# Optimization experiments

Hardware: AMD Instinct MI355X
Metric: run time of the kernel (lower is better)

## Reference

```python
import jax, jax.numpy as jnp
import numpy as np

B, N, R, NF, NH = 2, 2048, 16384, 128, 3
PSTEP = 3


def _lin(x, w, b):
    return x @ w + b


def _mlp2(x, w0, b0, w1, b1):
    return jax.nn.relu(_lin(jax.nn.relu(_lin(x, w0, b0)), w1, b1))


def setup_inputs() -> dict:
    key = jax.random.key(0)
    ks = jax.random.split(key, 16)

    def w(k, i, o):
        return (jax.random.normal(k, (i, o), dtype=jnp.float32) / np.float32(np.sqrt(i)))

    a_cur = jax.random.uniform(ks[0], (B, N), dtype=jnp.float32)
    s_cur = jax.random.normal(ks[1], (B, N, 3), dtype=jnp.float32)
    s_delta = jax.random.normal(ks[2], (B, NH, N, 3), dtype=jnp.float32)
    # Rr/Rs: dense one-hot receiver/sender matrices (B, rel_num, N)
    Rr = jax.nn.one_hot(jax.random.randint(ks[3], (B, R), 0, N), N, dtype=jnp.float32)
    Rs = jax.nn.one_hot(jax.random.randint(ks[4], (B, R), 0, N), N, dtype=jnp.float32)
    edge_attrs = (jax.random.uniform(ks[5], (B, R, 1)) > 0.5).astype(jnp.float32)
    z = lambda n: jnp.zeros((n,), dtype=jnp.float32)
    return {
        "a_cur": a_cur, "s_cur": s_cur, "s_delta": s_delta,
        "Rr": Rr, "Rs": Rs, "edge_attrs": edge_attrs,
        "pe_w0": w(ks[6], 3 * NH + 1, NF), "pe_b0": z(NF),
        "pe_w1": w(ks[7], NF, NF), "pe_b1": z(NF),
        "re_w0": w(ks[8], 6, NF), "re_b0": z(NF),
        "re_w1": w(ks[9], NF, NF), "re_b1": z(NF),
        "re_w2": w(ks[10], NF, NF), "re_b2": z(NF),
        "rp_w": w(ks[11], 3 * NF, NF), "rp_b": z(NF),
        "pp_w": w(ks[12], 2 * NF, NF), "pp_b": z(NF),
        "pr_w0": w(ks[13], NF, NF), "pr_b0": z(NF),
        "pr_w1": w(ks[14], NF, 3), "pr_b1": z(3),
    }


def reference(a_cur, s_cur, s_delta, Rr, Rs, edge_attrs,
              pe_w0, pe_b0, pe_w1, pe_b1,
              re_w0, re_b0, re_w1, re_b1, re_w2, re_b2,
              rp_w, rp_b, pp_w, pp_b,
              pr_w0, pr_b0, pr_w1, pr_b1):
    b, nh, n, _ = s_delta.shape
    # (B, n_history, N, 3) -> (B, N, 3*n_history)
    s_delta_flat = jnp.transpose(s_delta, (0, 2, 1, 3)).reshape(b, n, -1)
    a_r = jnp.einsum('brn,bn->br', Rr, a_cur)[..., None]
    a_s = jnp.einsum('brn,bn->br', Rs, a_cur)[..., None]
    s_r = jnp.einsum('brn,bnd->brd', Rr, s_cur)
    s_s = jnp.einsum('brn,bnd->brd', Rs, s_cur)

    particle_encode = _mlp2(jnp.concatenate([s_delta_flat, a_cur[..., None]], -1),
                            pe_w0, pe_b0, pe_w1, pe_b1)
    rel_in = jnp.concatenate([a_r, a_s, s_r - s_s, edge_attrs], -1)
    relation_encode = jax.nn.relu(_lin(
        jax.nn.relu(_lin(jax.nn.relu(_lin(rel_in, re_w0, re_b0)), re_w1, re_b1)),
        re_w2, re_b2))

    effect = particle_encode
    for _ in range(PSTEP):
        e_r = jnp.einsum('brn,bnf->brf', Rr, effect)
        e_s = jnp.einsum('brn,bnf->brf', Rs, effect)
        e_rel = jax.nn.relu(_lin(jnp.concatenate([relation_encode, e_r, e_s], -1), rp_w, rp_b))
        agg = jnp.einsum('brn,brf->bnf', Rr, e_rel)  # Rr^T aggregation
        effect = jax.nn.relu(
            _lin(jnp.concatenate([particle_encode, agg], -1), pp_w, pp_b) + effect)

    pred = _lin(jax.nn.relu(_lin(effect, pr_w0, pr_b0)), pr_w1, pr_b1)
    return pred + s_cur
```

## Files before the change

kernel.cpp:

```cpp
#include <hip/hip_runtime.h>
#include <hip/hip_bf16.h>
#include <stdint.h>

#define B_ 2
#define N_ 2048
#define R_ 16384
#define NF_ 128
#define NH_ 3
#define PSTEP_ 3
#define EDGES (B_ * R_)
#define NODES (B_ * N_)
#define PREP_EXB0 1024

typedef _Float16 f16;
typedef _Float16 f16x4 __attribute__((ext_vector_type(4)));
typedef float f32x4 __attribute__((ext_vector_type(4)));

struct GemmLds { f16 Ah[128 * 128], Al[128 * 128], Bh[128 * 128], Bl[128 * 128]; };
struct VecLds {
  float wbuf[64][NF_];
  float xt[NF_][20];
  float ht[NF_][20];
  float w0s[10][NF_];
  float b0s[NF_], b1s[NF_];
  float xs[16][10];
  float w1s[NF_][4];
};
union MainLds { GemmLds g; VecLds v; };

__device__ __forceinline__ void gl16(const f16* g, f16* l) {
  typedef const __attribute__((address_space(1))) uint32_t* gas_t;
  typedef __attribute__((address_space(3))) uint32_t* las_t;
  __builtin_amdgcn_global_load_lds((gas_t)(const void*)g, (las_t)(void*)l, 16, 0, 0);
}

__device__ __forceinline__ void mfma_block(const f16* Ah, const f16* Al,
                                           const f16* Bh, const f16* Bl,
                                           f32x4 (&acc)[8][2], int lane, int w) {
  const int l16 = lane & 15, l4 = lane >> 4;
  #pragma unroll 1
  for (int kk = 0; kk < 8; ++kk) {
    const int c16 = kk * 2 + (l4 >> 1);
    const int sub = (l4 & 1) * 4;
    f16x4 bh[2], bl[2];
    #pragma unroll
    for (int nf = 0; nf < 2; ++nf) {
      const int n = w * 32 + nf * 16 + l16;
      const int off = n * 128 + ((c16 ^ (n & 7)) * 8) + sub;
      bh[nf] = *(const f16x4*)&Bh[off];
      bl[nf] = *(const f16x4*)&Bl[off];
    }
    #pragma unroll
    for (int m = 0; m < 8; ++m) {
      const int r = m * 16 + l16;
      const int off = r * 128 + ((c16 ^ (r & 7)) * 8) + sub;
      const f16x4 ah = *(const f16x4*)&Ah[off];
      const f16x4 al = *(const f16x4*)&Al[off];
      #pragma unroll
      for (int nf = 0; nf < 2; ++nf) {
        acc[m][nf] = __builtin_amdgcn_mfma_f32_16x16x16f16(ah, bh[nf], acc[m][nf], 0, 0, 0);
        acc[m][nf] = __builtin_amdgcn_mfma_f32_16x16x16f16(ah, bl[nf], acc[m][nf], 0, 0, 0);
        acc[m][nf] = __builtin_amdgcn_mfma_f32_16x16x16f16(al, bh[nf], acc[m][nf], 0, 0, 0);
      }
    }
  }
}

__device__ __forceinline__ void frags_to_lds(f32x4 (&acc)[8][2], f16* Ah, f16* Al,
                                             int lane, int w) {
  const int l16 = lane & 15, l4 = lane >> 4;
  #pragma unroll
  for (int m = 0; m < 8; ++m)
    #pragma unroll
    for (int nf = 0; nf < 2; ++nf)
      #pragma unroll
      for (int i = 0; i < 4; ++i) {
        const float v = fmaxf(acc[m][nf][i], 0.f);
        const int row = m * 16 + l4 * 4 + i;
        const int col = w * 32 + nf * 16 + l16;
        const int off = row * 128 + (((col >> 3) ^ (row & 7)) * 8) + (col & 7);
        const f16 h = (f16)v;
        Ah[off] = h; Al[off] = (f16)(v - (float)h);
      }
}

__global__ __launch_bounds__(256) void k_prep(
    const float* __restrict__ Rr, const float* __restrict__ Rs,
    const float* __restrict__ rp_w, const float* __restrict__ re_w1,
    const float* __restrict__ re_w2,
    int* __restrict__ recv, int* __restrict__ send,
    f16* __restrict__ rpT_h, f16* __restrict__ rpT_l,
    f16* __restrict__ re1T_h, f16* __restrict__ re1T_l,
    f16* __restrict__ re2T_h, f16* __restrict__ re2T_l,
    float4* __restrict__ agg4) {
  const int bid = blockIdx.x, t = threadIdx.x;
  if (bid < 512) {
    agg4[bid * 256 + t] = make_float4(0.f, 0.f, 0.f, 0.f);
  } else if (bid >= 513 && bid < 833) {
    const int i = (bid - 513) * 256 + t;
    const int S1 = 384 * 128, S2 = S1 + 128 * 128, S3 = S2 + 128 * 128;
    if (i < S1) {
      const int k = i >> 7, n = i & 127;
      const float v = rp_w[i];
      const f16 h = (f16)v;
      rpT_h[n * 384 + k] = h; rpT_l[n * 384 + k] = (f16)(v - (float)h);
    } else if (i < S2) {
      const int j = i - S1, k = j >> 7, n = j & 127;
      const float v = re_w1[j];
      const f16 h = (f16)v;
      re1T_h[n * 128 + k] = h; re1T_l[n * 128 + k] = (f16)(v - (float)h);
    } else if (i < S3) {
      const int j = i - S2, k = j >> 7, n = j & 127;
      const float v = re_w2[j];
      const f16 h = (f16)v;
      re2T_h[n * 128 + k] = h; re2T_l[n * 128 + k] = (f16)(v - (float)h);
    }
  } else if (bid >= PREP_EXB0) {
    const int wid = (bid - PREP_EXB0) * 4 + (t >> 6);
    const int lane = t & 63;
    const bool isR = wid < EDGES;
    const int row = isR ? wid : wid - EDGES;
    const float4* p = reinterpret_cast<const float4*>((isR ? Rr : Rs) + (size_t)row * N_);
    int found = 0;
    #pragma unroll 1
    for (int it = 0; it < N_ / 256; ++it) {
      const float4 v = p[it * 64 + lane];
      const int base = (it * 64 + lane) * 4;
      bool hit = false;
      if (v.x != 0.f) { found = base;     hit = true; }
      if (v.y != 0.f) { found = base + 1; hit = true; }
      if (v.z != 0.f) { found = base + 2; hit = true; }
      if (v.w != 0.f) { found = base + 3; hit = true; }
      if (__any(hit)) break;
    }
    #pragma unroll
    for (int off = 32; off > 0; off >>= 1)
      found = max(found, __shfl_down(found, off, 64));
    if (lane == 0) (isR ? recv : send)[row] = found;
  }
}

__global__ __launch_bounds__(256, 1) void k_pre(
    const float* __restrict__ a_cur, const float* __restrict__ s_cur,
    const float* __restrict__ s_delta, const float* __restrict__ ea,
    const int* __restrict__ recv, const int* __restrict__ send,
    const float* __restrict__ pe_w0, const float* __restrict__ pe_b0,
    const float* __restrict__ pe_w1, const float* __restrict__ pe_b1,
    const float* __restrict__ re_w0, const float* __restrict__ re_b0,
    const float* __restrict__ re_b1, const float* __restrict__ re_b2,
    const f16* __restrict__ re1T_h, const f16* __restrict__ re1T_l,
    const f16* __restrict__ re2T_h, const f16* __restrict__ re2T_l,
    float* __restrict__ pe, f16* __restrict__ pe_h, f16* __restrict__ pe_l,
    f16* __restrict__ rel_h, f16* __restrict__ rel_l) {
  __shared__ MainLds u;
  __shared__ float xt6[6][128];
  __shared__ float w0s6[6][128];
  __shared__ float sb0[128];

  const int bid = blockIdx.x, t = threadIdx.x;
  const int lane = t & 63, w = t >> 6;
  const int l16 = lane & 15, l4 = lane >> 4;
  const int f = t & 127, g = t >> 7;

  auto stageB = [&](const f16* gh, const f16* gl) {
    #pragma unroll
    for (int rb = 0; rb < 32; rb += 4) {
      const int r0w = w * 32 + rb;
      const int row = r0w + l4;
      const int sc = (l16 ^ (row & 7)) * 8;
      gl16(gh + (size_t)row * 128 + sc, &u.g.Bh[r0w * 128]);
      gl16(gl + (size_t)row * 128 + sc, &u.g.Bl[r0w * 128]);
    }
  };

  {
    const int r0 = bid * 16;
    for (int i = t; i < 10 * NF_; i += 256) u.v.w0s[i >> 7][i & 127] = pe_w0[i];
    if (t < NF_) { u.v.b0s[t] = pe_b0[t]; u.v.b1s[t] = pe_b1[t]; }
    for (int i = t; i < 160; i += 256) {
      const int r = i / 10, k = i % 10;
      const int gr = r0 + r, b = gr >> 11, n = gr & (N_ - 1);
      u.v.xs[r][k] = (k < 9)
          ? s_delta[(((size_t)b * NH_ + (k / 3)) * N_ + n) * 3 + (k % 3)]
          : a_cur[gr];
    }
    __syncthreads();
    for (int r = g * 8; r < g * 8 + 8; ++r) {
      float a1 = u.v.b0s[f];
      #pragma unroll
      for (int k = 0; k < 10; ++k) a1 = fmaf(u.v.xs[r][k], u.v.w0s[k][f], a1);
      u.v.ht[f][r] = fmaxf(a1, 0.f);
    }
    float acc[8];
    #pragma unroll
    for (int i = 0; i < 8; ++i) acc[i] = u.v.b1s[f];
    for (int h = 0; h < 2; ++h) {
      __syncthreads();
      for (int i = t; i < 64 * NF_; i += 256) u.v.wbuf[i >> 7][i & 127] = pe_w1[h * 64 * NF_ + i];
      __syncthreads();
      for (int k = 0; k < 64; ++k) {
        const float wv = u.v.wbuf[k][f];
        #pragma unroll
        for (int i = 0; i < 2; ++i) {
          const float4 x4 = *reinterpret_cast<const float4*>(&u.v.ht[h * 64 + k][g * 8 + i * 4]);
          acc[i*4+0] = fmaf(x4.x, wv, acc[i*4+0]);
          acc[i*4+1] = fmaf(x4.y, wv, acc[i*4+1]);
          acc[i*4+2] = fmaf(x4.z, wv, acc[i*4+2]);
          acc[i*4+3] = fmaf(x4.w, wv, acc[i*4+3]);
        }
      }
    }
    #pragma unroll
    for (int i = 0; i < 8; ++i) {
      const size_t idx = (size_t)(r0 + g * 8 + i) * NF_ + f;
      const float v = fmaxf(acc[i], 0.f);
      pe[idx] = v;
      const f16 h = (f16)v;
      pe_h[idx] = h; pe_l[idx] = (f16)(v - (float)h);
    }
  }
  __syncthreads();

  {
    const int e0 = bid * 128;
    if (t < 128) {
      const int ge = e0 + t, b = ge >> 14;
      const int rc = recv[ge], sd = send[ge];
      xt6[0][t] = a_cur[(b << 11) + rc];
      xt6[1][t] = a_cur[(b << 11) + sd];
      #pragma unroll
      for (int d = 0; d < 3; ++d)
        xt6[2 + d][t] = s_cur[(size_t)((b << 11) + rc) * 3 + d]
                      - s_cur[(size_t)((b << 11) + sd) * 3 + d];
      xt6[5][t] = ea[ge];
    }
    stageB(re1T_h, re1T_l);
    for (int i = t; i < 6 * 128; i += 256) w0s6[i >> 7][i & 127] = re_w0[i];
    if (t < 128) sb0[t] = re_b0[t];
    __syncthreads();
    {
      float wreg[6];
      #pragma unroll
      for (int k = 0; k < 6; ++k) wreg[k] = w0s6[k][f];
      const float b0v = sb0[f];
      for (int r = g * 64; r < g * 64 + 64; ++r) {
        float a1 = b0v;
        #pragma unroll
        for (int k = 0; k < 6; ++k) a1 = fmaf(xt6[k][r], wreg[k], a1);
        a1 = fmaxf(a1, 0.f);
        const int off = r * 128 + ((((f >> 3)) ^ (r & 7)) * 8) + (f & 7);
        const f16 h = (f16)a1;
        u.g.Ah[off] = h; u.g.Al[off] = (f16)(a1 - (float)h);
      }
    }
    __syncthreads();
    f32x4 acc[8][2];
    {
      const float bv0 = re_b1[w * 32 + l16], bv1 = re_b1[w * 32 + 16 + l16];
      #pragma unroll
      for (int m = 0; m < 8; ++m) {
        acc[m][0] = (f32x4){bv0, bv0, bv0, bv0};
        acc[m][1] = (f32x4){bv1, bv1, bv1, bv1};
      }
    }
    mfma_block(u.g.Ah, u.g.Al, u.g.Bh, u.g.Bl, acc, lane, w);
    __syncthreads();
    frags_to_lds(acc, u.g.Ah, u.g.Al, lane, w);
    stageB(re2T_h, re2T_l);
    {
      const float bv0 = re_b2[w * 32 + l16], bv1 = re_b2[w * 32 + 16 + l16];
      #pragma unroll
      for (int m = 0; m < 8; ++m) {
        acc[m][0] = (f32x4){bv0, bv0, bv0, bv0};
        acc[m][1] = (f32x4){bv1, bv1, bv1, bv1};
      }
    }
    __syncthreads();
    mfma_block(u.g.Ah, u.g.Al, u.g.Bh, u.g.Bl, acc, lane, w);
    __syncthreads();
    frags_to_lds(acc, u.g.Ah, u.g.Al, lane, w);
    __syncthreads();
    {
      const int row = t >> 1, hf = t & 1;
      const float4* sA = (const float4*)&u.g.Ah[row * 128 + hf * 64];
      const float4* sL = (const float4*)&u.g.Al[row * 128 + hf * 64];
      float4* dA = (float4*)&rel_h[(size_t)(e0 + row) * 128 + hf * 64];
      float4* dL = (float4*)&rel_l[(size_t)(e0 + row) * 128 + hf * 64];
      #pragma unroll
      for (int j = 0; j < 8; ++j) { dA[j] = sA[j]; dL[j] = sL[j]; }
    }
  }
}

__global__ __launch_bounds__(256, 1) void k_erel(
    const f16* __restrict__ rel_h, const f16* __restrict__ rel_l,
    const f16* __restrict__ src_h, const f16* __restrict__ src_l,
    const int* __restrict__ recv, const int* __restrict__ send,
    const f16* __restrict__ rpT_h, const f16* __restrict__ rpT_l,
    const float* __restrict__ rp_b, float* __restrict__ agg) {
  __shared__ GemmLds u;
  __shared__ int eidx0[128], eidx1[128];
  const int bid = blockIdx.x, t = threadIdx.x;
  const int lane = t & 63, w = t >> 6;
  const int l16 = lane & 15, l4 = lane >> 4;
  const int e0 = bid * 128;
  const int b = bid >> 7;
  if (t < 128) eidx0[t] = recv[e0 + t];
  else         eidx1[t - 128] = send[e0 + t - 128];
  f32x4 acc[8][2];
  {
    const float bv0 = rp_b[w * 32 + l16], bv1 = rp_b[w * 32 + 16 + l16];
    #pragma unroll
    for (int m = 0; m < 8; ++m) {
      acc[m][0] = (f32x4){bv0, bv0, bv0, bv0};
      acc[m][1] = (f32x4){bv1, bv1, bv1, bv1};
    }
  }
  #pragma unroll 1
  for (int ch = 0; ch < 3; ++ch) {
    __syncthreads();
    #pragma unroll
    for (int rb = 0; rb < 32; rb += 4) {
      const int r0w = w * 32 + rb;
      const int row = r0w + l4;
      const int ge = e0 + row;
      if (ch == 0) {
        gl16(rel_h + (size_t)ge * 128 + l16 * 8, &u.Ah[r0w * 128]);
        gl16(rel_l + (size_t)ge * 128 + l16 * 8, &u.Al[r0w * 128]);
      } else {
        const int node = (ch == 1) ? eidx0[row] : eidx1[row];
        const size_t ao = ((size_t)(b << 11) + node) * 128 + ((l16 ^ (row & 7)) * 8);
        gl16(src_h + ao, &u.Ah[r0w * 128]);
        gl16(src_l + ao, &u.Al[r0w * 128]);
      }
      const int sc = (l16 ^ (row & 7)) * 8;
      gl16(rpT_h + (size_t)row * 384 + ch * 128 + sc, &u.Bh[r0w * 128]);
      gl16(rpT_l + (size_t)row * 384 + ch * 128 + sc, &u.Bl[r0w * 128]);
    }
    __syncthreads();
    mfma_block(u.Ah, u.Al, u.Bh, u.Bl, acc, lane, w);
  }
  #pragma unroll
  for (int m = 0; m < 8; ++m)
    #pragma unroll
    for (int nf = 0; nf < 2; ++nf)
      #pragma unroll
      for (int i = 0; i < 4; ++i) {
        const float v = fmaxf(acc[m][nf][i], 0.f);
        const int row = m * 16 + l4 * 4 + i;
        const int col = w * 32 + nf * 16 + l16;
        const int rc = eidx0[row];
        atomicAdd(&agg[((size_t)(b << 11) + rc) * NF_ + col], v);
      }
}

__global__ __launch_bounds__(256) void k_update(
    const float* __restrict__ pe, float* __restrict__ agg,
    const float* __restrict__ src_f,
    const float* __restrict__ pp_w, const float* __restrict__ pp_b,
    float* __restrict__ dst_f, f16* __restrict__ dst_h, f16* __restrict__ dst_l) {
  __shared__ alignas(16) float wbuf[64][NF_];
  __shared__ alignas(16) float xt[NF_][20];
  const int t = threadIdx.x, f = t & 127, g = t >> 7;
  const int r0 = blockIdx.x * 16;
  float acc[8];
  {
    const float bias = pp_b[f];
    #pragma unroll
    for (int i = 0; i < 8; ++i) acc[i] = bias;
  }
  for (int c = 0; c < 2; ++c) {
    __syncthreads();
    {
      const int e = t >> 4, k0 = (t & 15) * 8;
      float* srcp = (float*)((c ? agg : pe) + (size_t)(r0 + e) * NF_ + k0);
      #pragma unroll
      for (int j = 0; j < 2; ++j) {
        const float4 v = *reinterpret_cast<const float4*>(srcp + j * 4);
        xt[k0 + j*4 + 0][e] = v.x;
        xt[k0 + j*4 + 1][e] = v.y;
        xt[k0 + j*4 + 2][e] = v.z;
        xt[k0 + j*4 + 3][e] = v.w;
      }
      if (c == 1) {
        #pragma unroll
        for (int j = 0; j < 2; ++j)
          *reinterpret_cast<float4*>(srcp + j * 4) = make_float4(0.f, 0.f, 0.f, 0.f);
      }
    }
    #pragma unroll 1
    for (int h = 0; h < 2; ++h) {
      __syncthreads();
      for (int i = t; i < 64 * NF_; i += 256)
        wbuf[i >> 7][i & 127] = pp_w[(size_t)(c * NF_ + h * 64) * NF_ + i];
      __syncthreads();
      for (int k = 0; k < 64; ++k) {
        const float wv = wbuf[k][f];
        const int ka = h * 64 + k;
        #pragma unroll
        for (int i = 0; i < 2; ++i) {
          const float4 x4 = *reinterpret_cast<const float4*>(&xt[ka][g * 8 + i * 4]);
          acc[i*4+0] = fmaf(x4.x, wv, acc[i*4+0]);
          acc[i*4+1] = fmaf(x4.y, wv, acc[i*4+1]);
          acc[i*4+2] = fmaf(x4.z, wv, acc[i*4+2]);
          acc[i*4+3] = fmaf(x4.w, wv, acc[i*4+3]);
        }
      }
    }
  }
  #pragma unroll
  for (int i = 0; i < 8; ++i) {
    const size_t idx = (size_t)(r0 + g * 8 + i) * NF_ + f;
    const float v = fmaxf(acc[i] + src_f[idx], 0.f);
    dst_f[idx] = v;
    const f16 h = (f16)v;
    dst_h[idx] = h; dst_l[idx] = (f16)(v - (float)h);
  }
}

__global__ __launch_bounds__(256) void k_predict(
    const float* __restrict__ eff, const float* __restrict__ s_cur,
    const float* __restrict__ w0, const float* __restrict__ b0,
    const float* __restrict__ w1, const float* __restrict__ b1,
    float* __restrict__ out) {
  __shared__ alignas(16) float wbuf[64][NF_];
  __shared__ alignas(16) float xt[NF_][20];
  __shared__ alignas(16) float ht[NF_][20];
  __shared__ float w1s[NF_][4];
  const int t = threadIdx.x, f = t & 127, g = t >> 7;
  const int r0 = blockIdx.x * 16;
  for (int i = t; i < NF_ * 3; i += 256) w1s[i / 3][i % 3] = w1[i];
  {
    const int e = t >> 4, k0 = (t & 15) * 8;
    const float* src = eff + (size_t)(r0 + e) * NF_ + k0;
    #pragma unroll
    for (int j = 0; j < 2; ++j) {
      const float4 v = *reinterpret_cast<const float4*>(src + j * 4);
      xt[k0 + j*4 + 0][e] = v.x;
      xt[k0 + j*4 + 1][e] = v.y;
      xt[k0 + j*4 + 2][e] = v.z;
      xt[k0 + j*4 + 3][e] = v.w;
    }
  }
  float acc[8];
  {
    const float bias = b0[f];
    #pragma unroll
    for (int i = 0; i < 8; ++i) acc[i] = bias;
  }
  for (int h = 0; h < 2; ++h) {
    __syncthreads();
    for (int i = t; i < 64 * NF_; i += 256) wbuf[i >> 7][i & 127] = w0[h * 64 * NF_ + i];
    __syncthreads();
    for (int k = 0; k < 64; ++k) {
      const float wv = wbuf[k][f];
      const int ka = h * 64 + k;
      #pragma unroll
      for (int i = 0; i < 2; ++i) {
        const float4 x4 = *reinterpret_cast<const float4*>(&xt[ka][g * 8 + i * 4]);
        acc[i*4+0] = fmaf(x4.x, wv, acc[i*4+0]);
        acc[i*4+1] = fmaf(x4.y, wv, acc[i*4+1]);
        acc[i*4+2] = fmaf(x4.z, wv, acc[i*4+2]);
        acc[i*4+3] = fmaf(x4.w, wv, acc[i*4+3]);
      }
    }
  }
  #pragma unroll
  for (int i = 0; i < 8; ++i) ht[f][g * 8 + i] = fmaxf(acc[i], 0.f);
  __syncthreads();
  if (t < 48) {
    const int r = t / 3, d = t % 3;
    float a2 = b1[d];
    for (int k = 0; k < NF_; ++k) a2 = fmaf(ht[k][r], w1s[k][d], a2);
    const int gr = r0 + r;
    out[(size_t)gr * 3 + d] = a2 + s_cur[(size_t)gr * 3 + d];
  }
}

extern "C" void kernel_launch(void* const* d_in, const int* in_sizes, int n_in,
                              void* d_out, int out_size, void* d_ws, size_t ws_size,
                              hipStream_t stream) {
  (void)in_sizes; (void)n_in; (void)out_size; (void)ws_size;
  const float* a_cur   = (const float*)d_in[0];
  const float* s_cur   = (const float*)d_in[1];
  const float* s_delta = (const float*)d_in[2];
  const float* Rr      = (const float*)d_in[3];
  const float* Rs      = (const float*)d_in[4];
  const float* ea      = (const float*)d_in[5];
  const float* pe_w0 = (const float*)d_in[6];
  const float* pe_b0 = (const float*)d_in[7];
  const float* pe_w1 = (const float*)d_in[8];
  const float* pe_b1 = (const float*)d_in[9];
  const float* re_w0 = (const float*)d_in[10];
  const float* re_b0 = (const float*)d_in[11];
  const float* re_w1 = (const float*)d_in[12];
  const float* re_b1 = (const float*)d_in[13];
  const float* re_w2 = (const float*)d_in[14];
  const float* re_b2 = (const float*)d_in[15];
  const float* rp_w  = (const float*)d_in[16];
  const float* rp_b  = (const float*)d_in[17];
  const float* pp_w  = (const float*)d_in[18];
  const float* pp_b  = (const float*)d_in[19];
  const float* pr_w0 = (const float*)d_in[20];
  const float* pr_b0 = (const float*)d_in[21];
  const float* pr_w1 = (const float*)d_in[22];
  const float* pr_b1 = (const float*)d_in[23];
  float* out = (float*)d_out;

  uint8_t* wp = (uint8_t*)d_ws;
  auto alloc = [&](size_t bytes) {
    void* p = (void*)wp;
    wp += (bytes + 255) & ~(size_t)255;
    return p;
  };
  int* recv   = (int*)alloc(EDGES * 4);
  int* send   = (int*)alloc(EDGES * 4);
  float* pe   = (float*)alloc((size_t)NODES * NF_ * 4);
  f16* pe_h   = (f16*)alloc((size_t)NODES * NF_ * 2);
  f16* pe_l   = (f16*)alloc((size_t)NODES * NF_ * 2);
  float* eff  = (float*)alloc((size_t)NODES * NF_ * 4);
  f16* eff_h  = (f16*)alloc((size_t)NODES * NF_ * 2);
  f16* eff_l  = (f16*)alloc((size_t)NODES * NF_ * 2);
  float* agg  = (float*)alloc((size_t)NODES * NF_ * 4);
  f16* rel_h  = (f16*)alloc((size_t)EDGES * NF_ * 2);
  f16* rel_l  = (f16*)alloc((size_t)EDGES * NF_ * 2);
  f16* rpT_h  = (f16*)alloc(128 * 384 * 2);
  f16* rpT_l  = (f16*)alloc(128 * 384 * 2);
  f16* re1T_h = (f16*)alloc(128 * 128 * 2);
  f16* re1T_l = (f16*)alloc(128 * 128 * 2);
  f16* re2T_h = (f16*)alloc(128 * 128 * 2);
  f16* re2T_l = (f16*)alloc(128 * 128 * 2);

  k_prep<<<PREP_EXB0 + (2 * EDGES) / 4, 256, 0, stream>>>(
      Rr, Rs, rp_w, re_w1, re_w2, recv, send,
      rpT_h, rpT_l, re1T_h, re1T_l, re2T_h, re2T_l, (float4*)agg);

  k_pre<<<256, 256, 0, stream>>>(
      a_cur, s_cur, s_delta, ea, recv, send,
      pe_w0, pe_b0, pe_w1, pe_b1, re_w0, re_b0, re_b1, re_b2,
      re1T_h, re1T_l, re2T_h, re2T_l,
      pe, pe_h, pe_l, rel_h, rel_l);

  const float* esrc = pe;
  const f16* esrc_h = pe_h;
  const f16* esrc_l = pe_l;
  for (int s = 0; s < PSTEP_; ++s) {
    k_erel<<<EDGES / 128, 256, 0, stream>>>(rel_h, rel_l, esrc_h, esrc_l,
                                            recv, send, rpT_h, rpT_l, rp_b, agg);
    k_update<<<NODES / 16, 256, 0, stream>>>(pe, agg, esrc, pp_w, pp_b,
                                             eff, eff_h, eff_l);
    esrc = eff; esrc_h = eff_h; esrc_l = eff_l;
  }

  k_predict<<<NODES / 16, 256, 0, stream>>>(eff, s_cur, pr_w0, pr_b0,
                                            pr_w1, pr_b1, out);
}
```

Before: 702.1 us.

## Replace atomic scatter aggregation with receiver-bucket gather and fuse predict into final update

```diff
diff --git a/kernel.cpp b/kernel.cpp
--- a/kernel.cpp
+++ b/kernel.cpp
@@ -10,6 +10,7 @@
 #define PSTEP_ 3
 #define EDGES (B_ * R_)
 #define NODES (B_ * N_)
+#define MAXDEG 64
 #define PREP_EXB0 1024
 
 typedef _Float16 f16;
@@ -92,12 +93,12 @@
     f16* __restrict__ rpT_h, f16* __restrict__ rpT_l,
     f16* __restrict__ re1T_h, f16* __restrict__ re1T_l,
     f16* __restrict__ re2T_h, f16* __restrict__ re2T_l,
-    float4* __restrict__ agg4) {
+    int* __restrict__ counts) {
   const int bid = blockIdx.x, t = threadIdx.x;
-  if (bid < 512) {
-    agg4[bid * 256 + t] = make_float4(0.f, 0.f, 0.f, 0.f);
-  } else if (bid >= 513 && bid < 833) {
-    const int i = (bid - 513) * 256 + t;
+  if (bid < 16) {
+    counts[bid * 256 + t] = 0;
+  } else if (bid < 336) {
+    const int i = (bid - 16) * 256 + t;
     const int S1 = 384 * 128, S2 = S1 + 128 * 128, S3 = S2 + 128 * 128;
     if (i < S1) {
       const int k = i >> 7, n = i & 127;
@@ -151,7 +152,8 @@
     const f16* __restrict__ re1T_h, const f16* __restrict__ re1T_l,
     const f16* __restrict__ re2T_h, const f16* __restrict__ re2T_l,
     float* __restrict__ pe, f16* __restrict__ pe_h, f16* __restrict__ pe_l,
-    f16* __restrict__ rel_h, f16* __restrict__ rel_l) {
+    f16* __restrict__ rel_h, f16* __restrict__ rel_l,
+    int* __restrict__ counts, int* __restrict__ bucket) {
   __shared__ MainLds u;
   __shared__ float xt6[6][128];
   __shared__ float w0s6[6][128];
@@ -161,6 +163,15 @@
   const int lane = t & 63, w = t >> 6;
   const int l16 = lane & 15, l4 = lane >> 4;
   const int f = t & 127, g = t >> 7;
+
+  {
+    const int e = bid * 256 + t;
+    if (e < EDGES) {
+      const int gnode = (e >> 14) * N_ + recv[e];
+      const int pos = atomicAdd(&counts[gnode], 1);
+      if (pos < MAXDEG) bucket[gnode * MAXDEG + pos] = e;
+    }
+  }
 
   auto stageB = [&](const f16* gh, const f16* gl) {
     #pragma unroll
@@ -297,7 +308,7 @@
     const f16* __restrict__ src_h, const f16* __restrict__ src_l,
     const int* __restrict__ recv, const int* __restrict__ send,
     const f16* __restrict__ rpT_h, const f16* __restrict__ rpT_l,
-    const float* __restrict__ rp_b, float* __restrict__ agg) {
+    const float* __restrict__ rp_b, float* __restrict__ e_rel) {
   __shared__ GemmLds u;
   __shared__ int eidx0[128], eidx1[128];
   const int bid = blockIdx.x, t = threadIdx.x;
@@ -347,20 +358,26 @@
       #pragma unroll
       for (int i = 0; i < 4; ++i) {
         const float v = fmaxf(acc[m][nf][i], 0.f);
-        const int row = m * 16 + l4 * 4 + i;
+        const int row = e0 + m * 16 + l4 * 4 + i;
         const int col = w * 32 + nf * 16 + l16;
-        const int rc = eidx0[row];
-        atomicAdd(&agg[((size_t)(b << 11) + rc) * NF_ + col], v);
+        e_rel[(size_t)row * NF_ + col] = v;
       }
 }
 
 __global__ __launch_bounds__(256) void k_update(
-    const float* __restrict__ pe, float* __restrict__ agg,
+    const float* __restrict__ pe, const float* __restrict__ e_rel,
+    const int* __restrict__ counts, const int* __restrict__ bucket,
     const float* __restrict__ src_f,
     const float* __restrict__ pp_w, const float* __restrict__ pp_b,
-    float* __restrict__ dst_f, f16* __restrict__ dst_h, f16* __restrict__ dst_l) {
+    float* __restrict__ dst_f, f16* __restrict__ dst_h, f16* __restrict__ dst_l,
+    const float* __restrict__ s_cur,
+    const float* __restrict__ pr_w0, const float* __restrict__ pr_b0,
+    const float* __restrict__ pr_w1, const float* __restrict__ pr_b1,
+    float* __restrict__ out, int final_step) {
   __shared__ alignas(16) float wbuf[64][NF_];
   __shared__ alignas(16) float xt[NF_][20];
+  __shared__ alignas(16) float ht[NF_][20];
+  __shared__ float w1s[NF_][4];
   const int t = threadIdx.x, f = t & 127, g = t >> 7;
   const int r0 = blockIdx.x * 16;
   float acc[8];
@@ -373,20 +390,28 @@
     __syncthreads();
     {
       const int e = t >> 4, k0 = (t & 15) * 8;
-      float* srcp = (float*)((c ? agg : pe) + (size_t)(r0 + e) * NF_ + k0);
-      #pragma unroll
-      for (int j = 0; j < 2; ++j) {
-        const float4 v = *reinterpret_cast<const float4*>(srcp + j * 4);
-        xt[k0 + j*4 + 0][e] = v.x;
-        xt[k0 + j*4 + 1][e] = v.y;
-        xt[k0 + j*4 + 2][e] = v.z;
-        xt[k0 + j*4 + 3][e] = v.w;
-      }
-      if (c == 1) {
+      float s[8];
+      if (c == 0) {
+        const float* srcp = pe + (size_t)(r0 + e) * NF_ + k0;
+        const float4 v0 = *reinterpret_cast<const float4*>(srcp);
+        const float4 v1 = *reinterpret_cast<const float4*>(srcp + 4);
+        s[0]=v0.x; s[1]=v0.y; s[2]=v0.z; s[3]=v0.w;
+        s[4]=v1.x; s[5]=v1.y; s[6]=v1.z; s[7]=v1.w;
+      } else {
         #pragma unroll
-        for (int j = 0; j < 2; ++j)
-          *reinterpret_cast<float4*>(srcp + j * 4) = make_float4(0.f, 0.f, 0.f, 0.f);
-      }
+        for (int i = 0; i < 8; ++i) s[i] = 0.f;
+        const int gnode = r0 + e;
+        const int cnt = min(counts[gnode], MAXDEG);
+        for (int i = 0; i < cnt; ++i) {
+          const int ed = bucket[gnode * MAXDEG + i];
+          const float4 v0 = *reinterpret_cast<const float4*>(&e_rel[(size_t)ed * NF_ + k0]);
+          const float4 v1 = *reinterpret_cast<const float4*>(&e_rel[(size_t)ed * NF_ + k0 + 4]);
+          s[0]+=v0.x; s[1]+=v0.y; s[2]+=v0.z; s[3]+=v0.w;
+          s[4]+=v1.x; s[5]+=v1.y; s[6]+=v1.z; s[7]+=v1.w;
+        }
+      }
+      #pragma unroll
+      for (int i = 0; i < 8; ++i) xt[k0 + i][e] = s[i];
     }
     #pragma unroll 1
     for (int h = 0; h < 2; ++h) {
@@ -408,49 +433,32 @@
       }
     }
   }
+  if (!final_step) {
+    #pragma unroll
+    for (int i = 0; i < 8; ++i) {
+      const size_t idx = (size_t)(r0 + g * 8 + i) * NF_ + f;
+      const float v = fmaxf(acc[i] + src_f[idx], 0.f);
+      dst_f[idx] = v;
+      const f16 h = (f16)v;
+      dst_h[idx] = h; dst_l[idx] = (f16)(v - (float)h);
+    }
+    return;
+  }
+  __syncthreads();
   #pragma unroll
   for (int i = 0; i < 8; ++i) {
     const size_t idx = (size_t)(r0 + g * 8 + i) * NF_ + f;
-    const float v = fmaxf(acc[i] + src_f[idx], 0.f);
-    dst_f[idx] = v;
-    const f16 h = (f16)v;
-    dst_h[idx] = h; dst_l[idx] = (f16)(v - (float)h);
-  }
-}
-
-__global__ __launch_bounds__(256) void k_predict(
-    const float* __restrict__ eff, const float* __restrict__ s_cur,
-    const float* __restrict__ w0, const float* __restrict__ b0,
-    const float* __restrict__ w1, const float* __restrict__ b1,
-    float* __restrict__ out) {
-  __shared__ alignas(16) float wbuf[64][NF_];
-  __shared__ alignas(16) float xt[NF_][20];
-  __shared__ alignas(16) float ht[NF_][20];
-  __shared__ float w1s[NF_][4];
-  const int t = threadIdx.x, f = t & 127, g = t >> 7;
-  const int r0 = blockIdx.x * 16;
-  for (int i = t; i < NF_ * 3; i += 256) w1s[i / 3][i % 3] = w1[i];
+    xt[f][g * 8 + i] = fmaxf(acc[i] + src_f[idx], 0.f);
+  }
+  for (int i = t; i < NF_ * 3; i += 256) w1s[i / 3][i % 3] = pr_w1[i];
   {
-    const int e = t >> 4, k0 = (t & 15) * 8;
-    const float* src = eff + (size_t)(r0 + e) * NF_ + k0;
-    #pragma unroll
-    for (int j = 0; j < 2; ++j) {
-      const float4 v = *reinterpret_cast<const float4*>(src + j * 4);
-      xt[k0 + j*4 + 0][e] = v.x;
-      xt[k0 + j*4 + 1][e] = v.y;
-      xt[k0 + j*4 + 2][e] = v.z;
-      xt[k0 + j*4 + 3][e] = v.w;
-    }
-  }
-  float acc[8];
-  {
-    const float bias = b0[f];
+    const float bias = pr_b0[f];
     #pragma unroll
     for (int i = 0; i < 8; ++i) acc[i] = bias;
   }
   for (int h = 0; h < 2; ++h) {
     __syncthreads();
-    for (int i = t; i < 64 * NF_; i += 256) wbuf[i >> 7][i & 127] = w0[h * 64 * NF_ + i];
+    for (int i = t; i < 64 * NF_; i += 256) wbuf[i >> 7][i & 127] = pr_w0[h * 64 * NF_ + i];
     __syncthreads();
     for (int k = 0; k < 64; ++k) {
       const float wv = wbuf[k][f];
@@ -470,7 +478,7 @@
   __syncthreads();
   if (t < 48) {
     const int r = t / 3, d = t % 3;
-    float a2 = b1[d];
+    float a2 = pr_b1[d];
     for (int k = 0; k < NF_; ++k) a2 = fmaf(ht[k][r], w1s[k][d], a2);
     const int gr = r0 + r;
     out[(size_t)gr * 3 + d] = a2 + s_cur[(size_t)gr * 3 + d];
@@ -515,13 +523,18 @@
   };
   int* recv   = (int*)alloc(EDGES * 4);
   int* send   = (int*)alloc(EDGES * 4);
+  int* counts = (int*)alloc(NODES * 4);
+  int* bucket = (int*)alloc((size_t)NODES * MAXDEG * 4);
   float* pe   = (float*)alloc((size_t)NODES * NF_ * 4);
   f16* pe_h   = (f16*)alloc((size_t)NODES * NF_ * 2);
   f16* pe_l   = (f16*)alloc((size_t)NODES * NF_ * 2);
-  float* eff  = (float*)alloc((size_t)NODES * NF_ * 4);
-  f16* eff_h  = (f16*)alloc((size_t)NODES * NF_ * 2);
-  f16* eff_l  = (f16*)alloc((size_t)NODES * NF_ * 2);
-  float* agg  = (float*)alloc((size_t)NODES * NF_ * 4);
+  float* effA = (float*)alloc((size_t)NODES * NF_ * 4);
+  f16* effA_h = (f16*)alloc((size_t)NODES * NF_ * 2);
+  f16* effA_l = (f16*)alloc((size_t)NODES * NF_ * 2);
+  float* effB = (float*)alloc((size_t)NODES * NF_ * 4);
+  f16* effB_h = (f16*)alloc((size_t)NODES * NF_ * 2);
+  f16* effB_l = (f16*)alloc((size_t)NODES * NF_ * 2);
+  float* e_rel = (float*)alloc((size_t)EDGES * NF_ * 4);
   f16* rel_h  = (f16*)alloc((size_t)EDGES * NF_ * 2);
   f16* rel_l  = (f16*)alloc((size_t)EDGES * NF_ * 2);
   f16* rpT_h  = (f16*)alloc(128 * 384 * 2);
@@ -533,25 +546,26 @@
 
   k_prep<<<PREP_EXB0 + (2 * EDGES) / 4, 256, 0, stream>>>(
       Rr, Rs, rp_w, re_w1, re_w2, recv, send,
-      rpT_h, rpT_l, re1T_h, re1T_l, re2T_h, re2T_l, (float4*)agg);
+      rpT_h, rpT_l, re1T_h, re1T_l, re2T_h, re2T_l, counts);
 
   k_pre<<<256, 256, 0, stream>>>(
       a_cur, s_cur, s_delta, ea, recv, send,
       pe_w0, pe_b0, pe_w1, pe_b1, re_w0, re_b0, re_b1, re_b2,
       re1T_h, re1T_l, re2T_h, re2T_l,
-      pe, pe_h, pe_l, rel_h, rel_l);
+      pe, pe_h, pe_l, rel_h, rel_l, counts, bucket);
 
   const float* esrc = pe;
   const f16* esrc_h = pe_h;
   const f16* esrc_l = pe_l;
   for (int s = 0; s < PSTEP_; ++s) {
+    float* dst_f = (s == 1) ? effB   : effA;
+    f16*  dst_h  = (s == 1) ? effB_h : effA_h;
+    f16*  dst_l  = (s == 1) ? effB_l : effA_l;
     k_erel<<<EDGES / 128, 256, 0, stream>>>(rel_h, rel_l, esrc_h, esrc_l,
-                                            recv, send, rpT_h, rpT_l, rp_b, agg);
-    k_update<<<NODES / 16, 256, 0, stream>>>(pe, agg, esrc, pp_w, pp_b,
-                                             eff, eff_h, eff_l);
-    esrc = eff; esrc_h = eff_h; esrc_l = eff_l;
-  }
-
-  k_predict<<<NODES / 16, 256, 0, stream>>>(eff, s_cur, pr_w0, pr_b0,
-                                            pr_w1, pr_b1, out);
-}
+                                            recv, send, rpT_h, rpT_l, rp_b, e_rel);
+    k_update<<<NODES / 16, 256, 0, stream>>>(
+        pe, e_rel, counts, bucket, esrc, pp_w, pp_b, dst_f, dst_h, dst_l,
+        s_cur, pr_w0, pr_b0, pr_w1, pr_b1, out, (s == PSTEP_ - 1) ? 1 : 0);
+    esrc = dst_f; esrc_h = dst_h; esrc_l = dst_l;
+  }
+}
```

Result: no change. 692.5 us (-1.4%).
